# Optimization experiments

Measured on AMD Instinct MI355X. Metric: run time of the kernel, lower is better.

Reference implementation:

```python
import jax, jax.numpy as jnp
import numpy as np

# ---- fixed configuration (matches init_kwargs) ----
T, B, NIN, H, NOUT = 400, 256, 64, 512, 16
DT = 10.0                      # ms
DT_SEC = DT / 1000.0
ALPHA_NEURON = DT / 100.0      # dt / membrane_time_constant
NOISE_SD = 0.5
N_EXC = int(0.8 * H)
N_INH = H - N_EXC

_EI_SIGN = np.ones(H, dtype=np.float32)
_EI_SIGN[N_EXC:] = -1.0
# 'full' synapse config: alternating facilitating / depressing synapses
_idx = np.arange(H)
_FAC = (_idx % 2 == 0)
_U = np.where(_FAC, 0.15, 0.45).astype(np.float32)
_ALPHA_STF = np.where(_FAC, DT / 1500.0, DT / 200.0).astype(np.float32)  # dt/tau_u
_ALPHA_STD = np.where(_FAC, DT / 200.0, DT / 1500.0).astype(np.float32)  # dt/tau_x

EI_SIGN = jnp.asarray(_EI_SIGN)
U_VEC = jnp.asarray(_U)
ALPHA_STF = jnp.asarray(_ALPHA_STF)
ALPHA_STD = jnp.asarray(_ALPHA_STD)


def setup_inputs() -> dict:
    key = jax.random.key(0)
    k = jax.random.split(key, 6)
    x = jax.random.normal(k[0], (T, B, NIN), dtype=jnp.float32)
    # pre-sampled recurrent noise, scaled as sqrt(2*alpha)*noise_sd * N(0,1)
    noise = np.sqrt(2.0 * ALPHA_NEURON) * NOISE_SD * jax.random.normal(
        k[1], (T, B, H), dtype=jnp.float32)
    # gamma-like nonnegative initializations (abs-normal stand-in)
    W_in = jnp.abs(jax.random.normal(k[2], (NIN, H), dtype=jnp.float32)) * 0.05
    W_rnn = jnp.abs(jax.random.normal(k[3], (H, H), dtype=jnp.float32)) * 0.05
    b_rnn = jnp.zeros((H,), dtype=jnp.float32)
    W_out = jnp.abs(jax.random.normal(k[4], (H, NOUT), dtype=jnp.float32)) * 0.05
    W_out = W_out * jnp.asarray(np.concatenate(
        [np.ones((N_EXC, NOUT), np.float32), np.zeros((N_INH, NOUT), np.float32)]))
    b_out = jnp.zeros((NOUT,), dtype=jnp.float32)
    return {"x": x, "noise": noise, "W_in": W_in, "W_rnn": W_rnn,
            "b_rnn": b_rnn, "W_out": W_out, "b_out": b_out}


def reference(x, noise, W_in, W_rnn, b_rnn, W_out, b_out):
    # Dale's-law effective weights (sign applied to presynaptic rows)
    w_in_eff = jax.nn.relu(W_in)                       # [NIN, H]
    w_rnn_eff = jax.nn.relu(W_rnn) * EI_SIGN[:, None]  # [H, H]
    w_out_eff = jax.nn.relu(W_out)                     # [H, NOUT]

    h0 = 0.1 * jnp.ones((B, H), dtype=x.dtype)
    sx0 = jnp.ones((B, H), dtype=x.dtype)
    su0 = jnp.broadcast_to(U_VEC, (B, H)).astype(x.dtype)

    def step(carry, inp):
        h, syn_x, syn_u = carry
        x_t, n_t = inp
        # short-term plasticity dynamics
        syn_x = syn_x + ALPHA_STD * (1.0 - syn_x) - DT_SEC * syn_u * syn_x * h
        syn_u = syn_u + ALPHA_STF * (U_VEC - syn_u) + DT_SEC * U_VEC * (1.0 - syn_u) * h
        syn_x = jnp.clip(syn_x, 0.0, 1.0)
        syn_u = jnp.clip(syn_u, 0.0, 1.0)
        h_post = syn_u * syn_x * h
        # membrane dynamics with leaky integration + noise
        h = jax.nn.relu((1.0 - ALPHA_NEURON) * h
                        + ALPHA_NEURON * (x_t @ w_in_eff + h_post @ w_rnn_eff + b_rnn)
                        + n_t)
        logits = h @ w_out_eff + b_out
        return (h, syn_x, syn_u), (logits, h, syn_x, syn_u)

    _, (logits, h_seq, sx_seq, su_seq) = jax.lax.scan(step, (h0, sx0, su0), (x, noise))
    return logits, h_seq, sx_seq, su_seq
```

## Files before the change

### kernel.cpp

```cpp
#include <hip/hip_runtime.h>
#include <cstdint>

#define T_STEPS 400
#define B_SZ    256
#define NIN_SZ  64
#define H_SZ    512
#define NOUT_SZ 16
#define NEXC    409
#define MEMBERS 8
#define GROUPS  32
#define BG      8
#define CSL     64
#define NTHR    512
#define KEXT    576
#define KG      32
#define KR      18

#define WS_WRNN  0
#define WS_WIN   (H_SZ * H_SZ)
#define WS_WOUT  (WS_WIN + NIN_SZ * H_SZ)
#define WS_FLAGS (WS_WOUT + H_SZ * NOUT_SZ)

#define LDS_FLOATS (KEXT * 8 + KG * 8 * 64 + 512 + 64)

__global__ void prep_weights(const float* __restrict__ W_in,
                             const float* __restrict__ W_rnn,
                             const float* __restrict__ W_out,
                             float* __restrict__ ws) {
    int idx = blockIdx.x * blockDim.x + threadIdx.x;
    const int n_rnn = H_SZ * H_SZ;
    const int n_in  = NIN_SZ * H_SZ;
    const int n_out = H_SZ * NOUT_SZ;
    if (idx < n_rnn) {
        int k = idx >> 9;
        float v = fmaxf(W_rnn[idx], 0.0f);
        ws[idx] = (k < NEXC) ? v : -v;
    } else if (idx < n_rnn + n_in) {
        ws[idx] = fmaxf(W_in[idx - n_rnn], 0.0f);
    } else if (idx < n_rnn + n_in + n_out) {
        ws[idx] = fmaxf(W_out[idx - n_rnn - n_in], 0.0f);
    }
}

__global__ void zero_flags(unsigned int* __restrict__ flags) {
    if (threadIdx.x < MEMBERS * GROUPS) flags[threadIdx.x] = 0u;
}

#define FMA4(a, w, s)            \
    a.x = fmaf(w.x, s, a.x);     \
    a.y = fmaf(w.y, s, a.y);     \
    a.z = fmaf(w.z, s, a.z);     \
    a.w = fmaf(w.w, s, a.w);

__global__ __launch_bounds__(NTHR, 2)
void biornn_main(const float* __restrict__ x,
                 const float* __restrict__ noise,
                 const float* __restrict__ wrnn,
                 const float* __restrict__ win,
                 const float* __restrict__ brnn,
                 unsigned int* __restrict__ flags,
                 float* __restrict__ out_h,
                 float* __restrict__ out_sx,
                 float* __restrict__ out_su) {
    extern __shared__ float smem[];
    float* hpT    = smem;
    float* pbuf   = smem + KEXT * 8;
    float* h_own  = pbuf + KG * 8 * 64;
    float* brnn_l = h_own + 512;

    const int tid = threadIdx.x;
    const int bid = blockIdx.x;
    const int m   = bid >> 5;
    const int g   = bid & 31;
    const int c0  = m * CSL;
    const int b0  = g * BG;

    const int kg  = tid >> 4;
    const int ccg = tid & 15;
    const int cb  = tid >> 6;
    const int cc  = tid & 63;

    float4 Wv[KR];
#pragma unroll
    for (int i = 0; i < KR; ++i) {
        const int k = kg * KR + i;
        const float* src = (k < H_SZ)
            ? &wrnn[(size_t)k * H_SZ + c0 + ccg * 4]
            : &win[(size_t)(k - H_SZ) * H_SZ + c0 + ccg * 4];
        Wv[i] = *(const float4*)src;
    }
    if (tid < CSL) brnn_l[tid] = brnn[c0 + tid];
    h_own[tid] = 0.1f;

    const int j = tid;
    const bool  fac   = ((j & 1) == 0);
    const float Uj    = fac ? 0.15f : 0.45f;
    const float a_stf = fac ? (10.0f / 1500.0f) : (10.0f / 200.0f);
    const float a_std = fac ? (10.0f / 200.0f)  : (10.0f / 1500.0f);
    float hreg[8], sx[8], su[8];
#pragma unroll
    for (int r = 0; r < 8; ++r) { hreg[r] = 0.1f; sx[r] = 1.0f; su[r] = Uj; }
    const bool own = (j >= c0) && (j < c0 + CSL);
    __syncthreads();

    for (int t = 0; t < T_STEPS; ++t) {
        const float nz = noise[((size_t)t * B_SZ + b0 + cb) * H_SZ + c0 + cc];
        {
            float hp[8];
#pragma unroll
            for (int r = 0; r < 8; ++r) {
                float h_ = hreg[r], sx_ = sx[r], su_ = su[r];
                float sxn = sx_ + a_std * (1.0f - sx_) - 0.01f * su_ * sx_ * h_;
                float sun = su_ + a_stf * (Uj - su_)   + 0.01f * Uj * (1.0f - su_) * h_;
                sxn = fminf(fmaxf(sxn, 0.0f), 1.0f);
                sun = fminf(fmaxf(sun, 0.0f), 1.0f);
                sx[r] = sxn; su[r] = sun; hp[r] = sun * sxn * h_;
            }
            ((float4*)hpT)[j * 2]     = make_float4(hp[0], hp[1], hp[2], hp[3]);
            ((float4*)hpT)[j * 2 + 1] = make_float4(hp[4], hp[5], hp[6], hp[7]);
        }
        if (own) {
            const size_t ob = ((size_t)t * B_SZ + b0) * H_SZ + j;
#pragma unroll
            for (int r = 0; r < 8; ++r) {
                out_sx[ob + (size_t)r * H_SZ] = sx[r];
                out_su[ob + (size_t)r * H_SZ] = su[r];
            }
        }
        if (tid < NIN_SZ) {
#pragma unroll
            for (int r = 0; r < 8; ++r)
                hpT[(H_SZ + tid) * 8 + r] =
                    x[((size_t)t * B_SZ + b0 + r) * NIN_SZ + tid];
        }
        __syncthreads();

        float4 acc[8];
#pragma unroll
        for (int r = 0; r < 8; ++r) acc[r] = make_float4(0.f, 0.f, 0.f, 0.f);
        {
            const float4* hp4 = (const float4*)hpT;
            const int kbase = kg * KR;
#pragma unroll
            for (int i = 0; i < KR; ++i) {
                const float4 L  = hp4[(kbase + i) * 2];
                const float4 Hh = hp4[(kbase + i) * 2 + 1];
                const float4 w  = Wv[i];
                FMA4(acc[0], w, L.x)  FMA4(acc[1], w, L.y)
                FMA4(acc[2], w, L.z)  FMA4(acc[3], w, L.w)
                FMA4(acc[4], w, Hh.x) FMA4(acc[5], w, Hh.y)
                FMA4(acc[6], w, Hh.z) FMA4(acc[7], w, Hh.w)
            }
        }
#pragma unroll
        for (int r = 0; r < 8; ++r)
            *(float4*)&pbuf[(kg * 8 + r) * 64 + ccg * 4] = acc[r];
        __syncthreads();

        {
            float s = brnn_l[cc];
#pragma unroll
            for (int q = 0; q < KG; ++q)
                s += pbuf[(q * 8 + cb) * 64 + cc];
            const float hn =
                fmaxf(0.9f * h_own[cb * 64 + cc] + 0.1f * s + nz, 0.0f);
            h_own[cb * 64 + cc] = hn;
            float* hp_ = out_h + ((size_t)t * B_SZ + b0 + cb) * H_SZ + c0 + cc;
            asm volatile("global_store_dword %0, %1, off sc0 sc1"
                         :: "v"(hp_), "v"(hn) : "memory");
        }

        if (t == T_STEPS - 1) break;

        asm volatile("s_waitcnt vmcnt(0)" ::: "memory");
        __syncthreads();
        if (tid == 0) {
            unsigned int* fp = &flags[bid];
            unsigned int  tv = (unsigned)(t + 1);
            asm volatile("global_store_dword %0, %1, off sc0 sc1"
                         :: "v"(fp), "v"(tv) : "memory");
        }
        if (tid < MEMBERS) {
            const unsigned int want = (unsigned)(t + 1);
            unsigned int* fp = &flags[tid * GROUPS + g];
            unsigned int v;
            while (true) {
                asm volatile("global_load_dword %0, %1, off sc0 sc1\n\t"
                             "s_waitcnt vmcnt(0)"
                             : "=v"(v) : "v"(fp) : "memory");
                if (v >= want) break;
                __builtin_amdgcn_s_sleep(2);
            }
        }
        __syncthreads();
        {
            const float* q0 = out_h + ((size_t)t * B_SZ + b0) * H_SZ + j;
            const float* q2 = q0 + 2 * H_SZ;
            const float* q4 = q0 + 4 * H_SZ;
            const float* q6 = q0 + 6 * H_SZ;
            float g0, g1, g2, g3, g4, g5, g6, g7;
            asm volatile(
                "global_load_dword %0, %8,  off sc0 sc1\n\t"
                "global_load_dword %1, %8,  off offset:2048 sc0 sc1\n\t"
                "global_load_dword %2, %9,  off sc0 sc1\n\t"
                "global_load_dword %3, %9,  off offset:2048 sc0 sc1\n\t"
                "global_load_dword %4, %10, off sc0 sc1\n\t"
                "global_load_dword %5, %10, off offset:2048 sc0 sc1\n\t"
                "global_load_dword %6, %11, off sc0 sc1\n\t"
                "global_load_dword %7, %11, off offset:2048 sc0 sc1\n\t"
                "s_waitcnt vmcnt(0)"
                : "=&v"(g0), "=&v"(g1), "=&v"(g2), "=&v"(g3),
                  "=&v"(g4), "=&v"(g5), "=&v"(g6), "=&v"(g7)
                : "v"(q0), "v"(q2), "v"(q4), "v"(q6)
                : "memory");
            hreg[0] = g0; hreg[1] = g1; hreg[2] = g2; hreg[3] = g3;
            hreg[4] = g4; hreg[5] = g5; hreg[6] = g6; hreg[7] = g7;
        }
    }
}

__global__ __launch_bounds__(256)
void logits_k(const float* __restrict__ h, const float* __restrict__ wout,
              const float* __restrict__ bout, float* __restrict__ out) {
    __shared__ float wl[H_SZ * 17];
    __shared__ float bl[NOUT_SZ];
    const int tid = threadIdx.x;
    for (int i = tid; i < H_SZ * NOUT_SZ; i += 256)
        wl[(i >> 4) * 17 + (i & 15)] = wout[i];
    if (tid < NOUT_SZ) bl[tid] = bout[tid];
    __syncthreads();
    const size_t row = (size_t)blockIdx.x * 16 + (tid >> 4);
    const int o = tid & 15;
    const float* hr = h + row * H_SZ;
    float s = bl[o];
#pragma unroll 8
    for (int jj = 0; jj < H_SZ; ++jj)
        s = fmaf(hr[jj], wl[jj * 17 + o], s);
    out[row * NOUT_SZ + o] = s;
}

extern "C" void kernel_launch(void* const* d_in, const int* in_sizes, int n_in,
                              void* d_out, int out_size, void* d_ws, size_t ws_size,
                              hipStream_t stream) {
    const float* x     = (const float*)d_in[0];
    const float* noise = (const float*)d_in[1];
    const float* W_in  = (const float*)d_in[2];
    const float* W_rnn = (const float*)d_in[3];
    const float* b_rnn = (const float*)d_in[4];
    const float* W_out = (const float*)d_in[5];
    const float* b_out = (const float*)d_in[6];

    float* ws       = (float*)d_ws;
    float* wrnn_eff = ws + WS_WRNN;
    float* win_eff  = ws + WS_WIN;
    float* wout_eff = ws + WS_WOUT;
    unsigned int* flags = (unsigned int*)(ws + WS_FLAGS);

    float* out_logits = (float*)d_out;
    float* out_h  = out_logits + (size_t)T_STEPS * B_SZ * NOUT_SZ;
    float* out_sx = out_h  + (size_t)T_STEPS * B_SZ * H_SZ;
    float* out_su = out_sx + (size_t)T_STEPS * B_SZ * H_SZ;

    const int total = H_SZ * H_SZ + NIN_SZ * H_SZ + H_SZ * NOUT_SZ;
    prep_weights<<<(total + 255) / 256, 256, 0, stream>>>(W_in, W_rnn, W_out, ws);
    zero_flags<<<1, 256, 0, stream>>>(flags);

    biornn_main<<<MEMBERS * GROUPS, NTHR, LDS_FLOATS * sizeof(float), stream>>>(
        x, noise, wrnn_eff, win_eff, b_rnn, flags, out_h, out_sx, out_su);

    logits_k<<<(T_STEPS * B_SZ) / 16, 256, 0, stream>>>(
        out_h, wout_eff, b_out, out_logits);
}
```

Before: 2.911 ms.

## Replace flag barrier with tagged per-value exchange and finer batch split

Blocks now exchange presynaptic values h_post through tagged 64-bit slots, double-buffered in the logits output region. Each consumer polls until the tag for the current step appears, which replaces the per-block flag barrier and the separate reload of h. The batch per block drops from 8 to 4 to allow 512 blocks, partial sums are reduced across lanes with shuffles instead of LDS, and the weight preprocessing and flag-zeroing kernels are folded into the main kernel. The risks are heavier polling traffic, tags that could collide with stale data across calls, and the assumption that all 512 blocks stay co-resident.

```diff
diff --git a/kernel.cpp b/kernel.cpp
--- a/kernel.cpp
+++ b/kernel.cpp
@@ -8,75 +8,46 @@
 #define NOUT_SZ 16
 #define NEXC    409
 #define MEMBERS 8
-#define GROUPS  32
-#define BG      8
+#define BG      4
 #define CSL     64
 #define NTHR    512
+#define NBLK    512
 #define KEXT    576
-#define KG      32
 #define KR      18
-
-#define WS_WRNN  0
-#define WS_WIN   (H_SZ * H_SZ)
-#define WS_WOUT  (WS_WIN + NIN_SZ * H_SZ)
-#define WS_FLAGS (WS_WOUT + H_SZ * NOUT_SZ)
-
-#define LDS_FLOATS (KEXT * 8 + KG * 8 * 64 + 512 + 64)
-
-__global__ void prep_weights(const float* __restrict__ W_in,
-                             const float* __restrict__ W_rnn,
-                             const float* __restrict__ W_out,
-                             float* __restrict__ ws) {
-    int idx = blockIdx.x * blockDim.x + threadIdx.x;
-    const int n_rnn = H_SZ * H_SZ;
-    const int n_in  = NIN_SZ * H_SZ;
-    const int n_out = H_SZ * NOUT_SZ;
-    if (idx < n_rnn) {
-        int k = idx >> 9;
-        float v = fmaxf(W_rnn[idx], 0.0f);
-        ws[idx] = (k < NEXC) ? v : -v;
-    } else if (idx < n_rnn + n_in) {
-        ws[idx] = fmaxf(W_in[idx - n_rnn], 0.0f);
-    } else if (idx < n_rnn + n_in + n_out) {
-        ws[idx] = fmaxf(W_out[idx - n_rnn - n_in], 0.0f);
-    }
-}
-
-__global__ void zero_flags(unsigned int* __restrict__ flags) {
-    if (threadIdx.x < MEMBERS * GROUPS) flags[threadIdx.x] = 0u;
-}
-
-#define FMA4(a, w, s)            \
-    a.x = fmaf(w.x, s, a.x);     \
-    a.y = fmaf(w.y, s, a.y);     \
-    a.z = fmaf(w.z, s, a.z);     \
-    a.w = fmaf(w.w, s, a.w);
-
-__global__ __launch_bounds__(NTHR, 2)
+#define TAG_BASE 0x5A5A0000u
+
+#define RED4(a)                                                   \
+    a.x += __shfl_xor(a.x, 16); a.y += __shfl_xor(a.y, 16);       \
+    a.z += __shfl_xor(a.z, 16); a.w += __shfl_xor(a.w, 16);       \
+    a.x += __shfl_xor(a.x, 32); a.y += __shfl_xor(a.y, 32);       \
+    a.z += __shfl_xor(a.z, 32); a.w += __shfl_xor(a.w, 32);
+
+__global__ __launch_bounds__(NTHR, 4)
 void biornn_main(const float* __restrict__ x,
                  const float* __restrict__ noise,
-                 const float* __restrict__ wrnn,
-                 const float* __restrict__ win,
+                 const float* __restrict__ wrnn_raw,
+                 const float* __restrict__ win_raw,
                  const float* __restrict__ brnn,
-                 unsigned int* __restrict__ flags,
+                 uint64_t* __restrict__ hpx,
                  float* __restrict__ out_h,
                  float* __restrict__ out_sx,
-                 float* __restrict__ out_su) {
-    extern __shared__ float smem[];
-    float* hpT    = smem;
-    float* pbuf   = smem + KEXT * 8;
-    float* h_own  = pbuf + KG * 8 * 64;
-    float* brnn_l = h_own + 512;
+                 float* __restrict__ out_su)
+{
+    __shared__ __align__(16) float hpT[KEXT * BG];
+    __shared__ __align__(16) float pbuf[8 * BG * 64];
+    __shared__ float brnn_l[CSL];
 
     const int tid = threadIdx.x;
     const int bid = blockIdx.x;
-    const int m   = bid >> 5;
-    const int g   = bid & 31;
+    const int m   = bid & 7;
+    const int g   = bid >> 3;
     const int c0  = m * CSL;
     const int b0  = g * BG;
 
     const int kg  = tid >> 4;
-    const int ccg = tid & 15;
+    const int cg4 = (tid & 15) * 4;
+    const int wv  = tid >> 6;
+    const bool owner = (tid < BG * CSL);
     const int cb  = tid >> 6;
     const int cc  = tid & 63;
 
@@ -85,148 +56,152 @@
     for (int i = 0; i < KR; ++i) {
         const int k = kg * KR + i;
         const float* src = (k < H_SZ)
-            ? &wrnn[(size_t)k * H_SZ + c0 + ccg * 4]
-            : &win[(size_t)(k - H_SZ) * H_SZ + c0 + ccg * 4];
-        Wv[i] = *(const float4*)src;
+            ? &wrnn_raw[(size_t)k * H_SZ + c0 + cg4]
+            : &win_raw[(size_t)(k - H_SZ) * H_SZ + c0 + cg4];
+        float4 v = *(const float4*)src;
+        const float sgn = (k < H_SZ && k >= NEXC) ? -1.0f : 1.0f;
+        Wv[i] = make_float4(fmaxf(v.x, 0.0f) * sgn, fmaxf(v.y, 0.0f) * sgn,
+                            fmaxf(v.z, 0.0f) * sgn, fmaxf(v.w, 0.0f) * sgn);
     }
     if (tid < CSL) brnn_l[tid] = brnn[c0 + tid];
-    h_own[tid] = 0.1f;
-
-    const int j = tid;
-    const bool  fac   = ((j & 1) == 0);
+
+    const bool  fac   = ((tid & 1) == 0);
     const float Uj    = fac ? 0.15f : 0.45f;
     const float a_stf = fac ? (10.0f / 1500.0f) : (10.0f / 200.0f);
     const float a_std = fac ? (10.0f / 200.0f)  : (10.0f / 1500.0f);
-    float hreg[8], sx[8], su[8];
-#pragma unroll
-    for (int r = 0; r < 8; ++r) { hreg[r] = 0.1f; sx[r] = 1.0f; su[r] = Uj; }
-    const bool own = (j >= c0) && (j < c0 + CSL);
-    __syncthreads();
+
+    float h = 0.1f, sx, su;
+    {
+        const float sx0 = 1.0f, su0 = Uj;
+        float sxn = sx0 + a_std * (1.0f - sx0) - 0.01f * su0 * sx0 * h;
+        float sun = su0 + a_stf * (Uj - su0)   + 0.01f * Uj * (1.0f - su0) * h;
+        sx = fminf(fmaxf(sxn, 0.0f), 1.0f);
+        su = fminf(fmaxf(sun, 0.0f), 1.0f);
+        const float hp0 = su * sx * h;
+        ((float4*)hpT)[tid] = make_float4(hp0, hp0, hp0, hp0);
+        if (owner) {
+            const size_t ob = (size_t)(b0 + cb) * H_SZ + c0 + cc;
+            out_sx[ob] = sx;
+            out_su[ob] = su;
+        }
+    }
+    float xreg = 0.0f;
+    if (owner) xreg = x[(size_t)(b0 + cb) * NIN_SZ + cc];
 
     for (int t = 0; t < T_STEPS; ++t) {
-        const float nz = noise[((size_t)t * B_SZ + b0 + cb) * H_SZ + c0 + cc];
-        {
-            float hp[8];
-#pragma unroll
-            for (int r = 0; r < 8; ++r) {
-                float h_ = hreg[r], sx_ = sx[r], su_ = su[r];
-                float sxn = sx_ + a_std * (1.0f - sx_) - 0.01f * su_ * sx_ * h_;
-                float sun = su_ + a_stf * (Uj - su_)   + 0.01f * Uj * (1.0f - su_) * h_;
-                sxn = fminf(fmaxf(sxn, 0.0f), 1.0f);
-                sun = fminf(fmaxf(sun, 0.0f), 1.0f);
-                sx[r] = sxn; su[r] = sun; hp[r] = sun * sxn * h_;
-            }
-            ((float4*)hpT)[j * 2]     = make_float4(hp[0], hp[1], hp[2], hp[3]);
-            ((float4*)hpT)[j * 2 + 1] = make_float4(hp[4], hp[5], hp[6], hp[7]);
-        }
-        if (own) {
-            const size_t ob = ((size_t)t * B_SZ + b0) * H_SZ + j;
-#pragma unroll
-            for (int r = 0; r < 8; ++r) {
-                out_sx[ob + (size_t)r * H_SZ] = sx[r];
-                out_su[ob + (size_t)r * H_SZ] = su[r];
-            }
-        }
-        if (tid < NIN_SZ) {
-#pragma unroll
-            for (int r = 0; r < 8; ++r)
-                hpT[(H_SZ + tid) * 8 + r] =
-                    x[((size_t)t * B_SZ + b0 + r) * NIN_SZ + tid];
-        }
+        if (owner) hpT[(H_SZ + cc) * BG + cb] = xreg;
         __syncthreads();
 
-        float4 acc[8];
-#pragma unroll
-        for (int r = 0; r < 8; ++r) acc[r] = make_float4(0.f, 0.f, 0.f, 0.f);
+        float nz = 0.0f;
+        if (owner) nz = noise[((size_t)t * B_SZ + b0 + cb) * H_SZ + c0 + cc];
+
+        float4 a0 = make_float4(0.f, 0.f, 0.f, 0.f), a1 = a0, a2 = a0, a3 = a0;
         {
             const float4* hp4 = (const float4*)hpT;
-            const int kbase = kg * KR;
+            const int kb = kg * KR;
 #pragma unroll
             for (int i = 0; i < KR; ++i) {
-                const float4 L  = hp4[(kbase + i) * 2];
-                const float4 Hh = hp4[(kbase + i) * 2 + 1];
+                const float4 hv = hp4[kb + i];
                 const float4 w  = Wv[i];
-                FMA4(acc[0], w, L.x)  FMA4(acc[1], w, L.y)
-                FMA4(acc[2], w, L.z)  FMA4(acc[3], w, L.w)
-                FMA4(acc[4], w, Hh.x) FMA4(acc[5], w, Hh.y)
-                FMA4(acc[6], w, Hh.z) FMA4(acc[7], w, Hh.w)
+                a0.x = fmaf(w.x, hv.x, a0.x); a0.y = fmaf(w.y, hv.x, a0.y);
+                a0.z = fmaf(w.z, hv.x, a0.z); a0.w = fmaf(w.w, hv.x, a0.w);
+                a1.x = fmaf(w.x, hv.y, a1.x); a1.y = fmaf(w.y, hv.y, a1.y);
+                a1.z = fmaf(w.z, hv.y, a1.z); a1.w = fmaf(w.w, hv.y, a1.w);
+                a2.x = fmaf(w.x, hv.z, a2.x); a2.y = fmaf(w.y, hv.z, a2.y);
+                a2.z = fmaf(w.z, hv.z, a2.z); a2.w = fmaf(w.w, hv.z, a2.w);
+                a3.x = fmaf(w.x, hv.w, a3.x); a3.y = fmaf(w.y, hv.w, a3.y);
+                a3.z = fmaf(w.z, hv.w, a3.z); a3.w = fmaf(w.w, hv.w, a3.w);
             }
         }
-#pragma unroll
-        for (int r = 0; r < 8; ++r)
-            *(float4*)&pbuf[(kg * 8 + r) * 64 + ccg * 4] = acc[r];
+        if (owner && t + 1 < T_STEPS)
+            xreg = x[((size_t)(t + 1) * B_SZ + b0 + cb) * NIN_SZ + cc];
+
+        RED4(a0) RED4(a1) RED4(a2) RED4(a3)
+        if ((tid & 48) == 0) {
+            *(float4*)&pbuf[(wv * BG + 0) * 64 + cg4] = a0;
+            *(float4*)&pbuf[(wv * BG + 1) * 64 + cg4] = a1;
+            *(float4*)&pbuf[(wv * BG + 2) * 64 + cg4] = a2;
+            *(float4*)&pbuf[(wv * BG + 3) * 64 + cg4] = a3;
+        }
         __syncthreads();
 
-        {
+        if (owner) {
             float s = brnn_l[cc];
 #pragma unroll
-            for (int q = 0; q < KG; ++q)
-                s += pbuf[(q * 8 + cb) * 64 + cc];
-            const float hn =
-                fmaxf(0.9f * h_own[cb * 64 + cc] + 0.1f * s + nz, 0.0f);
-            h_own[cb * 64 + cc] = hn;
-            float* hp_ = out_h + ((size_t)t * B_SZ + b0 + cb) * H_SZ + c0 + cc;
-            asm volatile("global_store_dword %0, %1, off sc0 sc1"
-                         :: "v"(hp_), "v"(hn) : "memory");
-        }
-
-        if (t == T_STEPS - 1) break;
-
-        asm volatile("s_waitcnt vmcnt(0)" ::: "memory");
-        __syncthreads();
-        if (tid == 0) {
-            unsigned int* fp = &flags[bid];
-            unsigned int  tv = (unsigned)(t + 1);
-            asm volatile("global_store_dword %0, %1, off sc0 sc1"
-                         :: "v"(fp), "v"(tv) : "memory");
-        }
-        if (tid < MEMBERS) {
-            const unsigned int want = (unsigned)(t + 1);
-            unsigned int* fp = &flags[tid * GROUPS + g];
-            unsigned int v;
-            while (true) {
-                asm volatile("global_load_dword %0, %1, off sc0 sc1\n\t"
-                             "s_waitcnt vmcnt(0)"
-                             : "=v"(v) : "v"(fp) : "memory");
-                if (v >= want) break;
-                __builtin_amdgcn_s_sleep(2);
+            for (int q = 0; q < 8; ++q)
+                s += pbuf[(q * BG + cb) * 64 + cc];
+            const float hn = fmaxf(0.9f * h + 0.1f * s + nz, 0.0f);
+            out_h[((size_t)t * B_SZ + b0 + cb) * H_SZ + c0 + cc] = hn;
+            h = hn;
+            if (t + 1 < T_STEPS) {
+                float sxn = sx + a_std * (1.0f - sx) - 0.01f * su * sx * hn;
+                float sun = su + a_stf * (Uj - su)   + 0.01f * Uj * (1.0f - su) * hn;
+                sx = fminf(fmaxf(sxn, 0.0f), 1.0f);
+                su = fminf(fmaxf(sun, 0.0f), 1.0f);
+                const size_t ob = ((size_t)(t + 1) * B_SZ + b0 + cb) * H_SZ + c0 + cc;
+                out_sx[ob] = sx;
+                out_su[ob] = su;
+                const float hp = su * sx * hn;
+                const uint64_t pk =
+                    ((uint64_t)(TAG_BASE + (unsigned)(t + 1)) << 32) |
+                    (uint64_t)__float_as_uint(hp);
+                __hip_atomic_store(
+                    &hpx[((size_t)((t + 1) & 1) * B_SZ + b0 + cb) * H_SZ + c0 + cc],
+                    pk, __ATOMIC_RELAXED, __HIP_MEMORY_SCOPE_SYSTEM);
             }
         }
-        __syncthreads();
+        if (t + 1 >= T_STEPS) break;
+
         {
-            const float* q0 = out_h + ((size_t)t * B_SZ + b0) * H_SZ + j;
-            const float* q2 = q0 + 2 * H_SZ;
-            const float* q4 = q0 + 4 * H_SZ;
-            const float* q6 = q0 + 6 * H_SZ;
-            float g0, g1, g2, g3, g4, g5, g6, g7;
-            asm volatile(
-                "global_load_dword %0, %8,  off sc0 sc1\n\t"
-                "global_load_dword %1, %8,  off offset:2048 sc0 sc1\n\t"
-                "global_load_dword %2, %9,  off sc0 sc1\n\t"
-                "global_load_dword %3, %9,  off offset:2048 sc0 sc1\n\t"
-                "global_load_dword %4, %10, off sc0 sc1\n\t"
-                "global_load_dword %5, %10, off offset:2048 sc0 sc1\n\t"
-                "global_load_dword %6, %11, off sc0 sc1\n\t"
-                "global_load_dword %7, %11, off offset:2048 sc0 sc1\n\t"
-                "s_waitcnt vmcnt(0)"
-                : "=&v"(g0), "=&v"(g1), "=&v"(g2), "=&v"(g3),
-                  "=&v"(g4), "=&v"(g5), "=&v"(g6), "=&v"(g7)
-                : "v"(q0), "v"(q2), "v"(q4), "v"(q6)
-                : "memory");
-            hreg[0] = g0; hreg[1] = g1; hreg[2] = g2; hreg[3] = g3;
-            hreg[4] = g4; hreg[5] = g5; hreg[6] = g6; hreg[7] = g7;
+            const unsigned want = TAG_BASE + (unsigned)(t + 1);
+            uint64_t* slot = hpx + ((size_t)((t + 1) & 1) * B_SZ + b0) * H_SZ + tid;
+            unsigned done = 0;
+            float g0 = 0.f, g1 = 0.f, g2 = 0.f, g3 = 0.f;
+            while (__all(done == 15u) == 0) {
+                uint64_t v;
+                if (!(done & 1u)) {
+                    v = __hip_atomic_load(slot, __ATOMIC_RELAXED,
+                                          __HIP_MEMORY_SCOPE_SYSTEM);
+                    if ((unsigned)(v >> 32) == want) {
+                        g0 = __uint_as_float((unsigned)v); done |= 1u;
+                    }
+                }
+                if (!(done & 2u)) {
+                    v = __hip_atomic_load(slot + H_SZ, __ATOMIC_RELAXED,
+                                          __HIP_MEMORY_SCOPE_SYSTEM);
+                    if ((unsigned)(v >> 32) == want) {
+                        g1 = __uint_as_float((unsigned)v); done |= 2u;
+                    }
+                }
+                if (!(done & 4u)) {
+                    v = __hip_atomic_load(slot + 2 * H_SZ, __ATOMIC_RELAXED,
+                                          __HIP_MEMORY_SCOPE_SYSTEM);
+                    if ((unsigned)(v >> 32) == want) {
+                        g2 = __uint_as_float((unsigned)v); done |= 4u;
+                    }
+                }
+                if (!(done & 8u)) {
+                    v = __hip_atomic_load(slot + 3 * H_SZ, __ATOMIC_RELAXED,
+                                          __HIP_MEMORY_SCOPE_SYSTEM);
+                    if ((unsigned)(v >> 32) == want) {
+                        g3 = __uint_as_float((unsigned)v); done |= 8u;
+                    }
+                }
+                if (__all(done == 15u) == 0) __builtin_amdgcn_s_sleep(1);
+            }
+            ((float4*)hpT)[tid] = make_float4(g0, g1, g2, g3);
         }
     }
 }
 
 __global__ __launch_bounds__(256)
-void logits_k(const float* __restrict__ h, const float* __restrict__ wout,
+void logits_k(const float* __restrict__ h, const float* __restrict__ wout_raw,
               const float* __restrict__ bout, float* __restrict__ out) {
     __shared__ float wl[H_SZ * 17];
     __shared__ float bl[NOUT_SZ];
     const int tid = threadIdx.x;
     for (int i = tid; i < H_SZ * NOUT_SZ; i += 256)
-        wl[(i >> 4) * 17 + (i & 15)] = wout[i];
+        wl[(i >> 4) * 17 + (i & 15)] = fmaxf(wout_raw[i], 0.0f);
     if (tid < NOUT_SZ) bl[tid] = bout[tid];
     __syncthreads();
     const size_t row = (size_t)blockIdx.x * 16 + (tid >> 4);
@@ -250,24 +225,15 @@
     const float* W_out = (const float*)d_in[5];
     const float* b_out = (const float*)d_in[6];
 
-    float* ws       = (float*)d_ws;
-    float* wrnn_eff = ws + WS_WRNN;
-    float* win_eff  = ws + WS_WIN;
-    float* wout_eff = ws + WS_WOUT;
-    unsigned int* flags = (unsigned int*)(ws + WS_FLAGS);
-
     float* out_logits = (float*)d_out;
     float* out_h  = out_logits + (size_t)T_STEPS * B_SZ * NOUT_SZ;
     float* out_sx = out_h  + (size_t)T_STEPS * B_SZ * H_SZ;
     float* out_su = out_sx + (size_t)T_STEPS * B_SZ * H_SZ;
 
-    const int total = H_SZ * H_SZ + NIN_SZ * H_SZ + H_SZ * NOUT_SZ;
-    prep_weights<<<(total + 255) / 256, 256, 0, stream>>>(W_in, W_rnn, W_out, ws);
-    zero_flags<<<1, 256, 0, stream>>>(flags);
-
-    biornn_main<<<MEMBERS * GROUPS, NTHR, LDS_FLOATS * sizeof(float), stream>>>(
-        x, noise, wrnn_eff, win_eff, b_rnn, flags, out_h, out_sx, out_su);
-
+    uint64_t* hpx = (uint64_t*)out_logits;
+
+    biornn_main<<<NBLK, NTHR, 0, stream>>>(x, noise, W_rnn, W_in, b_rnn,
+                                           hpx, out_h, out_sx, out_su);
     logits_k<<<(T_STEPS * B_SZ) / 16, 256, 0, stream>>>(
-        out_h, wout_eff, b_out, out_logits);
+        out_h, W_out, b_out, out_logits);
 }
```

Measured after the change: 4.677 ms. 1.61x slower.
